# Performance work log

Hardware: AMD Instinct MI355X
Metric: run time of the kernel (lower is better)

The kernel has to match this reference:

```python
import jax, jax.numpy as jnp
import numpy as np

B, T, F, H, HORIZON = 16384, 50, 2, 64, 50


def setup_inputs() -> dict:
    key = jax.random.key(0)
    ks = jax.random.split(key, 7)
    s = 1.0 / np.sqrt(H)  # PyTorch LSTM init scale
    return {
        "history": jax.random.normal(ks[0], (B, T, F), jnp.float32),
        "W_ih": jax.random.uniform(ks[1], (4 * H, F), jnp.float32, -s, s),
        "W_hh": jax.random.uniform(ks[2], (4 * H, H), jnp.float32, -s, s),
        "b_ih": jax.random.uniform(ks[3], (4 * H,), jnp.float32, -s, s),
        "b_hh": jax.random.uniform(ks[4], (4 * H,), jnp.float32, -s, s),
        "W_dec": jax.random.uniform(ks[5], (F, H), jnp.float32, -s, s),
        "b_dec": jax.random.uniform(ks[6], (F,), jnp.float32, -s, s),
    }


def _lstm_cell(h, c, x, W_ih, W_hh, b):
    # gates in PyTorch order: input, forget, cell(g), output
    gates = x @ W_ih.T + h @ W_hh.T + b  # [B, 4H]
    i, f, g, o = jnp.split(gates, 4, axis=-1)
    c_new = jax.nn.sigmoid(f) * c + jax.nn.sigmoid(i) * jnp.tanh(g)
    h_new = jax.nn.sigmoid(o) * jnp.tanh(c_new)
    return h_new, c_new


def reference(history, W_ih, W_hh, b_ih, b_hh, W_dec, b_dec):
    b = b_ih + b_hh
    nb, hdim = history.shape[0], W_hh.shape[1]
    h0 = jnp.zeros((nb, hdim), history.dtype)
    c0 = jnp.zeros((nb, hdim), history.dtype)

    # Encode history: scan over time (xs leading axis = T)
    def enc_step(carry, x_t):
        h, c = carry
        h, c = _lstm_cell(h, c, x_t, W_ih, W_hh, b)
        return (h, c), None

    (h, c), _ = jax.lax.scan(enc_step, (h0, c0), jnp.swapaxes(history, 0, 1))

    x0 = history[:, -1, :]  # [B, F]

    def dec_step(carry, _):
        h, c, x = carry
        h, c = _lstm_cell(h, c, x, W_ih, W_hh, b)
        dxy = h @ W_dec.T + b_dec  # [B, F]
        return (h, c, dxy), dxy

    _, preds = jax.lax.scan(dec_step, (h, c, x0), None, length=HORIZON)
    return jnp.swapaxes(preds, 0, 1)  # [B, HORIZON, F]
```

## Files before the change

### kernel.cpp

```cpp
#include <hip/hip_runtime.h>

typedef __attribute__((ext_vector_type(8))) short short8;
typedef __attribute__((ext_vector_type(4))) float f32x4;
typedef __attribute__((ext_vector_type(2))) float f32x2;

#define TSTEPS 50
#define HOR    50

__device__ __forceinline__ float frcp(float x) { return __builtin_amdgcn_rcpf(x); }
__device__ __forceinline__ float sigmoidf(float x) { return frcp(1.f + __expf(-x)); }
__device__ __forceinline__ float tanh_fast(float x) {
  float ax = fabsf(x);
  float e  = __expf(-2.f * ax);
  float r  = (1.f - e) * frcp(1.f + e);
  return copysignf(r, x);
}
__device__ __forceinline__ unsigned cvt_pk_bf16(float a, float b) {
  unsigned r;
  asm("v_cvt_pk_bf16_f32 %0, %1, %2" : "=v"(r) : "v"(a), "v"(b));
  return r;
}
union S8U { short8 s; unsigned u[4]; };

__device__ __forceinline__ void split8(const float* f, short8& hi, short8& lo) {
  S8U h, l;
  #pragma unroll
  for (int e = 0; e < 4; ++e) {
    float a = f[2 * e], b = f[2 * e + 1];
    unsigned ph = cvt_pk_bf16(a, b);
    float ah = __uint_as_float(ph << 16);
    float bh = __uint_as_float(ph & 0xFFFF0000u);
    h.u[e] = ph;
    l.u[e] = cvt_pk_bf16(a - ah, b - bh);
  }
  hi = h.s; lo = l.s;
}

__global__ __launch_bounds__(256, 2)
void traj_lstm_mfma2(const float* __restrict__ hist,
                     const float* __restrict__ W_ih,
                     const float* __restrict__ W_hh,
                     const float* __restrict__ b_ih,
                     const float* __restrict__ b_hh,
                     const float* __restrict__ W_dec,
                     const float* __restrict__ b_dec,
                     float* __restrict__ out)
{
  __shared__ float hsh[2][2][16][68];
  __shared__ float xsh[2][16][2];
  __shared__ float wdl[2][64];

  const int tid  = threadIdx.x;
  const int w    = tid >> 6;
  const int lane = tid & 63;
  const int col  = lane & 15;
  const int g    = lane >> 4;
  const int pr   = w >> 1;
  const int p    = w & 1;
  const int batch0 = blockIdx.x * 32 + pr * 16;

  short8 wbhi[4][2][2], wblo[4][2][2];
  #pragma unroll
  for (int gt = 0; gt < 4; ++gt)
    #pragma unroll
    for (int u = 0; u < 2; ++u) {
      const int row = gt * 64 + (2 * p + u) * 16 + col;
      #pragma unroll
      for (int q = 0; q < 2; ++q) {
        float f[8];
        #pragma unroll
        for (int e = 0; e < 8; ++e) f[e] = W_hh[row * 64 + q * 32 + g * 8 + e];
        split8(f, wbhi[gt][u][q], wblo[gt][u][q]);
      }
    }

  float bias[4][2], wih0[4][2], wih1[4][2];
  #pragma unroll
  for (int gt = 0; gt < 4; ++gt)
    #pragma unroll
    for (int u = 0; u < 2; ++u) {
      const int row = gt * 64 + (2 * p + u) * 16 + col;
      bias[gt][u] = b_ih[row] + b_hh[row];
      wih0[gt][u] = W_ih[row * 2];
      wih1[gt][u] = W_ih[row * 2 + 1];
    }
  const float bdp = b_dec[p];

  if (tid < 128) wdl[tid >> 6][tid & 63] = W_dec[tid];
  for (int i = tid; i < 2 * 16 * 68; i += 256) ((float*)hsh[0])[i] = 0.f;

  float cst[4][2];
  #pragma unroll
  for (int r = 0; r < 4; ++r)
    #pragma unroll
    for (int u = 0; u < 2; ++u) cst[r][u] = 0.f;

  __syncthreads();

  for (int s = 0; s < TSTEPS + HOR; ++s) {
    const int par = s & 1;

    short8 ahi[2], alo[2];
    #pragma unroll
    for (int q = 0; q < 2; ++q) {
      float hf[8];
      *(f32x4*)&hf[0] = *(const f32x4*)&hsh[par][pr][col][q * 32 + g * 8];
      *(f32x4*)&hf[4] = *(const f32x4*)&hsh[par][pr][col][q * 32 + g * 8 + 4];
      split8(hf, ahi[q], alo[q]);
    }

    float x0[4], x1[4];
    if (s <= TSTEPS) {
      const int ss = (s < TSTEPS) ? s : (TSTEPS - 1);
      #pragma unroll
      for (int r = 0; r < 4; ++r) {
        f32x2 xv = *(const f32x2*)&hist[(size_t)(batch0 + 4 * g + r) * 100 + ss * 2];
        x0[r] = xv.x; x1[r] = xv.y;
      }
    } else {
      #pragma unroll
      for (int r = 0; r < 4; ++r) {
        f32x2 xv = *(const f32x2*)&xsh[pr][4 * g + r][0];
        x0[r] = xv.x; x1[r] = xv.y;
      }
    }

    f32x4 acc[4][2];
    #pragma unroll
    for (int gt = 0; gt < 4; ++gt)
      #pragma unroll
      for (int u = 0; u < 2; ++u) {
        f32x4 a = {0.f, 0.f, 0.f, 0.f};
        a = __builtin_amdgcn_mfma_f32_16x16x32_bf16(ahi[0], wbhi[gt][u][0], a, 0, 0, 0);
        a = __builtin_amdgcn_mfma_f32_16x16x32_bf16(ahi[1], wbhi[gt][u][1], a, 0, 0, 0);
        a = __builtin_amdgcn_mfma_f32_16x16x32_bf16(alo[0], wbhi[gt][u][0], a, 0, 0, 0);
        a = __builtin_amdgcn_mfma_f32_16x16x32_bf16(alo[1], wbhi[gt][u][1], a, 0, 0, 0);
        a = __builtin_amdgcn_mfma_f32_16x16x32_bf16(ahi[0], wblo[gt][u][0], a, 0, 0, 0);
        a = __builtin_amdgcn_mfma_f32_16x16x32_bf16(ahi[1], wblo[gt][u][1], a, 0, 0, 0);
        acc[gt][u] = a;
      }

    #pragma unroll
    for (int r = 0; r < 4; ++r)
      #pragma unroll
      for (int u = 0; u < 2; ++u) {
        float gi = acc[0][u][r] + bias[0][u] + x0[r] * wih0[0][u] + x1[r] * wih1[0][u];
        float gf = acc[1][u][r] + bias[1][u] + x0[r] * wih0[1][u] + x1[r] * wih1[1][u];
        float gg = acc[2][u][r] + bias[2][u] + x0[r] * wih0[2][u] + x1[r] * wih1[2][u];
        float go = acc[3][u][r] + bias[3][u] + x0[r] * wih0[3][u] + x1[r] * wih1[3][u];
        float si = sigmoidf(gi);
        float sf = sigmoidf(gf);
        float tg = tanh_fast(gg);
        float so = sigmoidf(go);
        float cn = fmaf(sf, cst[r][u], si * tg);
        cst[r][u] = cn;
        float hv = so * tanh_fast(cn);
        hsh[par ^ 1][pr][4 * g + r][(2 * p + u) * 16 + col] = hv;
      }
    __syncthreads();

    if (s >= TSTEPS) {
      const float* hr = &hsh[par ^ 1][pr][col][g * 16];
      const float* wr = &wdl[p][g * 16];
      float part = 0.f;
      #pragma unroll
      for (int e4 = 0; e4 < 4; ++e4) {
        f32x4 hv = *(const f32x4*)&hr[e4 * 4];
        f32x4 wv = *(const f32x4*)&wr[e4 * 4];
        part += hv.x * wv.x + hv.y * wv.y + hv.z * wv.z + hv.w * wv.w;
      }
      part += __shfl_xor(part, 16);
      part += __shfl_xor(part, 32);
      const float dxy = part + bdp;
      if (g == 0) {
        xsh[pr][col][p] = dxy;
        out[(size_t)(batch0 + col) * 100 + (size_t)(s - TSTEPS) * 2 + p] = dxy;
      }
      __syncthreads();
    }
  }
}

extern "C" void kernel_launch(void* const* d_in, const int* in_sizes, int n_in,
                              void* d_out, int out_size, void* d_ws, size_t ws_size,
                              hipStream_t stream) {
  (void)in_sizes; (void)n_in; (void)ws_size; (void)d_ws; (void)out_size;
  const float* hist  = (const float*)d_in[0];
  const float* W_ih  = (const float*)d_in[1];
  const float* W_hh  = (const float*)d_in[2];
  const float* b_ih  = (const float*)d_in[3];
  const float* b_hh  = (const float*)d_in[4];
  const float* W_dec = (const float*)d_in[5];
  const float* b_dec = (const float*)d_in[6];
  float* out = (float*)d_out;

  dim3 grid(16384 / 32);
  dim3 block(256);
  traj_lstm_mfma2<<<grid, block, 0, stream>>>(hist, W_ih, W_hh, b_ih, b_hh,
                                              W_dec, b_dec, out);
}
```

Baseline: 325.7 us.

## Split hidden units across four waves per 16-row batch tile, drop decoder barrier

Each block now handles 16 batch rows with four waves, each owning 16 hidden columns of every gate, which halves per-wave weight registers and accumulators and allows 4 blocks per CU. Every wave computes both decoder outputs redundantly and broadcasts the fed-back inputs through shuffles instead of shared memory, which removes the second per-step barrier in the decode phase. The trade-off is duplicated decoder dot products and twice as many blocks, with more barriers in total across blocks.

```diff
diff --git a/kernel.cpp b/kernel.cpp
--- a/kernel.cpp
+++ b/kernel.cpp
@@ -36,8 +36,8 @@
   hi = h.s; lo = l.s;
 }
 
-__global__ __launch_bounds__(256, 2)
-void traj_lstm_mfma2(const float* __restrict__ hist,
+__global__ __launch_bounds__(256, 4)
+void traj_lstm_mfma4(const float* __restrict__ hist,
                      const float* __restrict__ W_ih,
                      const float* __restrict__ W_hh,
                      const float* __restrict__ b_ih,
@@ -46,54 +46,44 @@
                      const float* __restrict__ b_dec,
                      float* __restrict__ out)
 {
-  __shared__ float hsh[2][2][16][68];
-  __shared__ float xsh[2][16][2];
+  __shared__ float hsh[2][16][68];
   __shared__ float wdl[2][64];
 
   const int tid  = threadIdx.x;
-  const int w    = tid >> 6;
+  const int q    = tid >> 6;
   const int lane = tid & 63;
   const int col  = lane & 15;
   const int g    = lane >> 4;
-  const int pr   = w >> 1;
-  const int p    = w & 1;
-  const int batch0 = blockIdx.x * 32 + pr * 16;
+  const int batch0 = blockIdx.x * 16;
 
-  short8 wbhi[4][2][2], wblo[4][2][2];
+  short8 wbhi[4][2], wblo[4][2];
   #pragma unroll
-  for (int gt = 0; gt < 4; ++gt)
+  for (int gt = 0; gt < 4; ++gt) {
+    const int row = gt * 64 + q * 16 + col;
     #pragma unroll
-    for (int u = 0; u < 2; ++u) {
-      const int row = gt * 64 + (2 * p + u) * 16 + col;
+    for (int kq = 0; kq < 2; ++kq) {
+      float f[8];
       #pragma unroll
-      for (int q = 0; q < 2; ++q) {
-        float f[8];
-        #pragma unroll
-        for (int e = 0; e < 8; ++e) f[e] = W_hh[row * 64 + q * 32 + g * 8 + e];
-        split8(f, wbhi[gt][u][q], wblo[gt][u][q]);
-      }
+      for (int e = 0; e < 8; ++e) f[e] = W_hh[row * 64 + kq * 32 + g * 8 + e];
+      split8(f, wbhi[gt][kq], wblo[gt][kq]);
     }
+  }
 
-  float bias[4][2], wih0[4][2], wih1[4][2];
+  float bias[4], wih0[4], wih1[4];
   #pragma unroll
-  for (int gt = 0; gt < 4; ++gt)
-    #pragma unroll
-    for (int u = 0; u < 2; ++u) {
-      const int row = gt * 64 + (2 * p + u) * 16 + col;
-      bias[gt][u] = b_ih[row] + b_hh[row];
-      wih0[gt][u] = W_ih[row * 2];
-      wih1[gt][u] = W_ih[row * 2 + 1];
-    }
-  const float bdp = b_dec[p];
+  for (int gt = 0; gt < 4; ++gt) {
+    const int row = gt * 64 + q * 16 + col;
+    bias[gt] = b_ih[row] + b_hh[row];
+    wih0[gt] = W_ih[row * 2];
+    wih1[gt] = W_ih[row * 2 + 1];
+  }
+  const float bd0 = b_dec[0], bd1 = b_dec[1];
 
   if (tid < 128) wdl[tid >> 6][tid & 63] = W_dec[tid];
-  for (int i = tid; i < 2 * 16 * 68; i += 256) ((float*)hsh[0])[i] = 0.f;
+  for (int i = tid; i < 16 * 68; i += 256) ((float*)hsh[0])[i] = 0.f;
 
-  float cst[4][2];
-  #pragma unroll
-  for (int r = 0; r < 4; ++r)
-    #pragma unroll
-    for (int u = 0; u < 2; ++u) cst[r][u] = 0.f;
+  float cst[4] = {0.f, 0.f, 0.f, 0.f};
+  float x0[4], x1[4];
 
   __syncthreads();
 
@@ -102,14 +92,13 @@
 
     short8 ahi[2], alo[2];
     #pragma unroll
-    for (int q = 0; q < 2; ++q) {
+    for (int kq = 0; kq < 2; ++kq) {
       float hf[8];
-      *(f32x4*)&hf[0] = *(const f32x4*)&hsh[par][pr][col][q * 32 + g * 8];
-      *(f32x4*)&hf[4] = *(const f32x4*)&hsh[par][pr][col][q * 32 + g * 8 + 4];
-      split8(hf, ahi[q], alo[q]);
+      *(f32x4*)&hf[0] = *(const f32x4*)&hsh[par][col][kq * 32 + g * 8];
+      *(f32x4*)&hf[4] = *(const f32x4*)&hsh[par][col][kq * 32 + g * 8 + 4];
+      split8(hf, ahi[kq], alo[kq]);
     }
 
-    float x0[4], x1[4];
     if (s <= TSTEPS) {
       const int ss = (s < TSTEPS) ? s : (TSTEPS - 1);
       #pragma unroll
@@ -117,66 +106,61 @@
         f32x2 xv = *(const f32x2*)&hist[(size_t)(batch0 + 4 * g + r) * 100 + ss * 2];
         x0[r] = xv.x; x1[r] = xv.y;
       }
-    } else {
-      #pragma unroll
-      for (int r = 0; r < 4; ++r) {
-        f32x2 xv = *(const f32x2*)&xsh[pr][4 * g + r][0];
-        x0[r] = xv.x; x1[r] = xv.y;
-      }
     }
 
-    f32x4 acc[4][2];
+    f32x4 acc[4];
     #pragma unroll
-    for (int gt = 0; gt < 4; ++gt)
-      #pragma unroll
-      for (int u = 0; u < 2; ++u) {
-        f32x4 a = {0.f, 0.f, 0.f, 0.f};
-        a = __builtin_amdgcn_mfma_f32_16x16x32_bf16(ahi[0], wbhi[gt][u][0], a, 0, 0, 0);
-        a = __builtin_amdgcn_mfma_f32_16x16x32_bf16(ahi[1], wbhi[gt][u][1], a, 0, 0, 0);
-        a = __builtin_amdgcn_mfma_f32_16x16x32_bf16(alo[0], wbhi[gt][u][0], a, 0, 0, 0);
-        a = __builtin_amdgcn_mfma_f32_16x16x32_bf16(alo[1], wbhi[gt][u][1], a, 0, 0, 0);
-        a = __builtin_amdgcn_mfma_f32_16x16x32_bf16(ahi[0], wblo[gt][u][0], a, 0, 0, 0);
-        a = __builtin_amdgcn_mfma_f32_16x16x32_bf16(ahi[1], wblo[gt][u][1], a, 0, 0, 0);
-        acc[gt][u] = a;
-      }
+    for (int gt = 0; gt < 4; ++gt) {
+      f32x4 a = {0.f, 0.f, 0.f, 0.f};
+      a = __builtin_amdgcn_mfma_f32_16x16x32_bf16(ahi[0], wbhi[gt][0], a, 0, 0, 0);
+      a = __builtin_amdgcn_mfma_f32_16x16x32_bf16(ahi[1], wbhi[gt][1], a, 0, 0, 0);
+      a = __builtin_amdgcn_mfma_f32_16x16x32_bf16(alo[0], wbhi[gt][0], a, 0, 0, 0);
+      a = __builtin_amdgcn_mfma_f32_16x16x32_bf16(alo[1], wbhi[gt][1], a, 0, 0, 0);
+      a = __builtin_amdgcn_mfma_f32_16x16x32_bf16(ahi[0], wblo[gt][0], a, 0, 0, 0);
+      a = __builtin_amdgcn_mfma_f32_16x16x32_bf16(ahi[1], wblo[gt][1], a, 0, 0, 0);
+      acc[gt] = a;
+    }
 
     #pragma unroll
-    for (int r = 0; r < 4; ++r)
-      #pragma unroll
-      for (int u = 0; u < 2; ++u) {
-        float gi = acc[0][u][r] + bias[0][u] + x0[r] * wih0[0][u] + x1[r] * wih1[0][u];
-        float gf = acc[1][u][r] + bias[1][u] + x0[r] * wih0[1][u] + x1[r] * wih1[1][u];
-        float gg = acc[2][u][r] + bias[2][u] + x0[r] * wih0[2][u] + x1[r] * wih1[2][u];
-        float go = acc[3][u][r] + bias[3][u] + x0[r] * wih0[3][u] + x1[r] * wih1[3][u];
-        float si = sigmoidf(gi);
-        float sf = sigmoidf(gf);
-        float tg = tanh_fast(gg);
-        float so = sigmoidf(go);
-        float cn = fmaf(sf, cst[r][u], si * tg);
-        cst[r][u] = cn;
-        float hv = so * tanh_fast(cn);
-        hsh[par ^ 1][pr][4 * g + r][(2 * p + u) * 16 + col] = hv;
-      }
+    for (int r = 0; r < 4; ++r) {
+      float gi = acc[0][r] + bias[0] + x0[r] * wih0[0] + x1[r] * wih1[0];
+      float gf = acc[1][r] + bias[1] + x0[r] * wih0[1] + x1[r] * wih1[1];
+      float gg = acc[2][r] + bias[2] + x0[r] * wih0[2] + x1[r] * wih1[2];
+      float go = acc[3][r] + bias[3] + x0[r] * wih0[3] + x1[r] * wih1[3];
+      float si = sigmoidf(gi);
+      float sf = sigmoidf(gf);
+      float tg = tanh_fast(gg);
+      float so = sigmoidf(go);
+      float cn = fmaf(sf, cst[r], si * tg);
+      cst[r] = cn;
+      hsh[par ^ 1][4 * g + r][q * 16 + col] = so * tanh_fast(cn);
+    }
     __syncthreads();
 
     if (s >= TSTEPS) {
-      const float* hr = &hsh[par ^ 1][pr][col][g * 16];
-      const float* wr = &wdl[p][g * 16];
-      float part = 0.f;
+      const float* hr = &hsh[par ^ 1][col][g * 16];
+      float p0 = 0.f, p1 = 0.f;
       #pragma unroll
       for (int e4 = 0; e4 < 4; ++e4) {
         f32x4 hv = *(const f32x4*)&hr[e4 * 4];
-        f32x4 wv = *(const f32x4*)&wr[e4 * 4];
-        part += hv.x * wv.x + hv.y * wv.y + hv.z * wv.z + hv.w * wv.w;
+        f32x4 w0 = *(const f32x4*)&wdl[0][g * 16 + e4 * 4];
+        f32x4 w1 = *(const f32x4*)&wdl[1][g * 16 + e4 * 4];
+        p0 += hv.x * w0.x + hv.y * w0.y + hv.z * w0.z + hv.w * w0.w;
+        p1 += hv.x * w1.x + hv.y * w1.y + hv.z * w1.z + hv.w * w1.w;
       }
-      part += __shfl_xor(part, 16);
-      part += __shfl_xor(part, 32);
-      const float dxy = part + bdp;
-      if (g == 0) {
-        xsh[pr][col][p] = dxy;
-        out[(size_t)(batch0 + col) * 100 + (size_t)(s - TSTEPS) * 2 + p] = dxy;
+      p0 += __shfl_xor(p0, 16); p0 += __shfl_xor(p0, 32);
+      p1 += __shfl_xor(p1, 16); p1 += __shfl_xor(p1, 32);
+      p0 += bd0; p1 += bd1;
+
+      if (q == 0 && g == 0) {
+        f32x2 o2 = { p0, p1 };
+        *(f32x2*)&out[(size_t)(batch0 + col) * 100 + (size_t)(s - TSTEPS) * 2] = o2;
       }
-      __syncthreads();
+      #pragma unroll
+      for (int r = 0; r < 4; ++r) {
+        x0[r] = __shfl(p0, 4 * g + r);
+        x1[r] = __shfl(p1, 4 * g + r);
+      }
     }
   }
 }
@@ -194,8 +178,8 @@
   const float* b_dec = (const float*)d_in[6];
   float* out = (float*)d_out;
 
-  dim3 grid(16384 / 32);
+  dim3 grid(16384 / 16);
   dim3 block(256);
-  traj_lstm_mfma2<<<grid, block, 0, stream>>>(hist, W_ih, W_hh, b_ih, b_hh,
+  traj_lstm_mfma4<<<grid, block, 0, stream>>>(hist, W_ih, W_hh, b_ih, b_hh,
                                               W_dec, b_dec, out);
 }
```

New measurement: 417.1 us. 1.28x slower.
